# Performance work log

Measured on AMD Instinct MI355X. Metric: run time of the kernel, lower is better.

The kernel has to match this reference:

```python
import math
import jax, jax.numpy as jnp
from jax import lax
import numpy as np

D = 256; H = 8; NL = 6; HALF = D // 2
B = 32; NEV = 256

def sinpos(x):
    # SinusoidalPosEmb: (..., ) int -> (..., D)
    freq = jnp.exp(jnp.arange(HALF, dtype=jnp.float32) * (-math.log(10000.0) / (HALF - 1)))
    e = x.astype(jnp.float32)[..., None] * freq
    return jnp.concatenate([jnp.sin(e), jnp.cos(e)], axis=-1)

def layer_norm(x, g, b, eps=1e-5):
    m = x.mean(-1, keepdims=True)
    v = ((x - m) ** 2).mean(-1, keepdims=True)
    return (x - m) / jnp.sqrt(v + eps) * g + b

def gelu(x):
    return jax.nn.gelu(x, approximate=False)

def conv1d(x, w, b, stride):
    y = lax.conv_general_dilated(x, w, (stride,), [(3, 3)], dimension_numbers=("NCH", "OIH", "NCH"))
    return y + b[None, :, None]

def setup_inputs():
    ks = iter(jax.random.split(jax.random.key(0), 48))
    def p(*shape):
        return jax.random.normal(next(ks), shape, dtype=jnp.float32) * 0.02
    inp = dict(
        mel=jax.random.normal(next(ks), (B, 80, 2000), dtype=jnp.float32),
        events=jnp.sort(jax.random.randint(next(ks), (B, NEV), 0, 2000), axis=-1),
        event_mask=jnp.zeros((B, NEV), dtype=bool),
        star_rating=jax.random.uniform(next(ks), (B,), dtype=jnp.float32) * 9.0,
        mel_W=p(16, 80), mel_b=p(16),
        conv1_w=p(128, 16, 7), conv1_b=p(128),
        gn_g=jnp.ones(128, jnp.float32), gn_b=jnp.zeros(128, jnp.float32),
        conv2_w=p(256, 128, 7), conv2_b=p(256),
        cn_g=jnp.ones(D, jnp.float32), cn_b=jnp.zeros(D, jnp.float32),
        star_table=p(20, D),
        ep_W1=p(D, 3 * D), ep_b1=p(D), ep_W2=p(D, D), ep_b2=p(D),
        tl_Wqkv=p(NL, 3 * D, D), tl_bqkv=p(NL, 3 * D),
        tl_Wo=p(NL, D, D), tl_bo=p(NL, D),
        tl_ln1g=jnp.ones((NL, D), jnp.float32), tl_ln1b=jnp.zeros((NL, D), jnp.float32),
        tl_ln2g=jnp.ones((NL, D), jnp.float32), tl_ln2b=jnp.zeros((NL, D), jnp.float32),
        tl_W1=p(NL, 4 * D, D), tl_b1=p(NL, 4 * D),
        tl_W2=p(NL, D, 4 * D), tl_b2=p(NL, D),
        pool_q=jax.random.normal(next(ks), (D,), dtype=jnp.float32),
        on_g=jnp.ones(D, jnp.float32), on_b=jnp.zeros(D, jnp.float32),
        oh_W=p(1, D), oh_b=p(1),
    )
    return inp

def reference(mel, events, event_mask, star_rating, mel_W, mel_b, conv1_w, conv1_b, gn_g, gn_b, conv2_w, conv2_b, cn_g, cn_b, star_table, ep_W1, ep_b1, ep_W2, ep_b2, tl_Wqkv, tl_bqkv, tl_Wo, tl_bo, tl_ln1g, tl_ln1b, tl_ln2g, tl_ln2b, tl_W1, tl_b1, tl_W2, tl_b2, pool_q, on_g, on_b, oh_W, oh_b):
    Bsz = mel.shape[0]
    # mel_compress on channel dim: (B,80,T) -> (B,16,T)
    x_mel = jnp.einsum('bct,oc->bot', mel, mel_W) + mel_b[None, :, None]
    h = gelu(conv1d(x_mel, conv1_w, conv1_b, 2))           # (B,128,1000)
    # GroupNorm(1, C): normalize over (C, L) per sample
    m = h.mean((1, 2), keepdims=True)
    v = ((h - m) ** 2).mean((1, 2), keepdims=True)
    h = (h - m) / jnp.sqrt(v + 1e-5) * gn_g[None, :, None] + gn_b[None, :, None]
    h = gelu(conv1d(h, conv2_w, conv2_b, 2))               # (B,256,500)
    x = h.transpose(0, 2, 1)                               # (B,500,256)
    x = layer_norm(x, cn_g, cn_b)
    S = x.shape[1]
    x = x + sinpos(jnp.arange(S))[None]
    star_bucket = jnp.clip((star_rating / 0.5).astype(jnp.int32), 0, star_table.shape[0] - 1)
    x = x + star_table[star_bucket][:, None, :]
    # --- event gap/ratio embeddings (vectorized; exact match to torch loop when all valid) ---
    diff = jnp.maximum(events[:, 1:] - events[:, :-1], 1)  # clamp(min=1)
    g = jnp.concatenate([diff[:, :1], diff], axis=1)        # g[0] = g[1]
    gap_ms = g * 5
    g_f = jnp.maximum(g.astype(jnp.float32), 1.0)
    r = jnp.clip(g_f[:, 1:] / g_f[:, :-1], 0.1, 10.0)
    ones = jnp.ones((Bsz, 1), dtype=jnp.float32)
    ratio_before = (jnp.concatenate([ones, r], axis=1) * 50).astype(jnp.int32)
    ratio_after = (jnp.concatenate([r, ones], axis=1) * 50).astype(jnp.int32)
    combined = jnp.concatenate([sinpos(ratio_before), sinpos(ratio_after), sinpos(gap_ms)], axis=-1)
    ev = gelu(combined @ ep_W1.T + ep_b1) @ ep_W2.T + ep_b2
    ev = jnp.where(event_mask[..., None], 0.0, ev)
    token_pos = jnp.clip(events // 4, 0, S - 1)
    # batched scatter-add of event embeddings into token stream
    x = x.at[jnp.arange(Bsz)[:, None], token_pos].add(ev)
    hd = D // H
    for i in range(NL):
        xn = layer_norm(x, tl_ln1g[i], tl_ln1b[i])
        qkv = xn @ tl_Wqkv[i].T + tl_bqkv[i]
        q, k, vv = jnp.split(qkv, 3, axis=-1)
        q = q.reshape(Bsz, S, H, hd).transpose(0, 2, 1, 3)
        k = k.reshape(Bsz, S, H, hd).transpose(0, 2, 1, 3)
        vv = vv.reshape(Bsz, S, H, hd).transpose(0, 2, 1, 3)
        a = jax.nn.softmax(jnp.einsum('bhqd,bhkd->bhqk', q, k) / math.sqrt(hd), axis=-1)
        o = jnp.einsum('bhqk,bhkd->bhqd', a, vv).transpose(0, 2, 1, 3).reshape(Bsz, S, D)
        x = x + o @ tl_Wo[i].T + tl_bo[i]
        xn = layer_norm(x, tl_ln2g[i], tl_ln2b[i])
        x = x + gelu(xn @ tl_W1[i].T + tl_b1[i]) @ tl_W2[i].T + tl_b2[i]
    # attention pooling + head
    logits = x @ pool_q / math.sqrt(D)
    w = jax.nn.softmax(logits, axis=-1)
    pooled = jnp.einsum('bs,bsd->bd', w, x)
    return (layer_norm(pooled, on_g, on_b) @ oh_W.T + oh_b).squeeze(-1)
```

## Files before the change

kernel.cpp:

```cpp
#include <hip/hip_runtime.h>
#include <math.h>

namespace {
constexpr int kB = 32;
constexpr int kS = 500;
constexpr int kH = 8;
}
#define LKC (-0.07252236513366287)

typedef __attribute__((ext_vector_type(8))) short s16x8;
typedef __attribute__((ext_vector_type(4))) float f32x4;

__device__ __forceinline__ float gelu_f(float x){
  return 0.5f * x * (1.0f + erff(x * 0.7071067811865476f));
}
__device__ __forceinline__ float b2f(short s){
  union { unsigned u; float f; } x; x.u = ((unsigned)(unsigned short)s) << 16; return x.f;
}
__device__ __forceinline__ short f2b(float f){
  unsigned u = __float_as_uint(f);
  unsigned r = (u + 0x7fffu + ((u >> 16) & 1u)) >> 16;
  return (short)r;
}
__device__ __forceinline__ unsigned cvtpk(float lo, float hi){
  unsigned r;
  asm("v_cvt_pk_bf16_f32 %0, %1, %2" : "=v"(r) : "v"(lo), "v"(hi));
  return r;
}

__global__ __launch_bounds__(128) void conv1w_pad(const float* __restrict__ w, short* __restrict__ out){
  int n = blockIdx.x, k = threadIdx.x;
  out[n*128 + k] = (k < 112) ? f2b(w[n*112 + k]) : (short)0;
}

__global__ __launch_bounds__(256) void f2b_all(const float* __restrict__ c2,
    const float* __restrict__ e1, const float* __restrict__ e2,
    const float* __restrict__ qk, const float* __restrict__ wo,
    const float* __restrict__ w1, const float* __restrict__ w2,
    short* __restrict__ WB){
  int blk = blockIdx.x, t = threadIdx.x;
  const float* src; short* dst; int idx;
  if(blk < 896){        src = c2; dst = WB + 16384;   idx = blk*256 + t; }
  else if(blk < 1664){  src = e1; dst = WB + 245760;  idx = (blk-896)*256 + t; }
  else if(blk < 1920){  src = e2; dst = WB + 442368;  idx = (blk-1664)*256 + t; }
  else if(blk < 6528){  src = qk; dst = WB + 507904;  idx = (blk-1920)*256 + t; }
  else if(blk < 8064){  src = wo; dst = WB + 1687552; idx = (blk-6528)*256 + t; }
  else if(blk < 14208){ src = w1; dst = WB + 2080768; idx = (blk-8064)*256 + t; }
  else {                src = w2; dst = WB + 3653632; idx = (blk-14208)*256 + t; }
  dst[idx] = f2b(src[idx]);
}

template<int OUT, bool DOGELU>
__global__ __launch_bounds__(256) void gemm_mfma(const short* __restrict__ A,
    const short* __restrict__ W, const float* __restrict__ bias,
    void* __restrict__ Cv, int M, int N, int K){
  __shared__ __align__(16) short Al[128*64];
  __shared__ __align__(16) short Wl[128*64];
  const int t = threadIdx.x;
  const int wid = t >> 6, lane = t & 63;
  const int m0 = blockIdx.y * 128, n0 = blockIdx.x * 128;
  const int wr = (wid >> 1) * 64, wc = (wid & 1) * 64;
  const int frow = lane & 15, lg = lane >> 4;
  const int rA = t >> 3;
  const int sA = (t & 7) ^ (rA & 7);
  const short* Aq = A + (size_t)(m0 + rA) * K + sA * 8;
  const short* Wq = W + (size_t)(n0 + rA) * K + sA * 8;
  f32x4 acc[4][4] = {};
  for(int k0 = 0; k0 < K; k0 += 64){
    s16x8 av[4], wv[4];
    #pragma unroll
    for(int j = 0; j < 4; ++j){
      av[j] = *(const s16x8*)(Aq + k0 + (size_t)(32*j)*K);
      wv[j] = *(const s16x8*)(Wq + k0 + (size_t)(32*j)*K);
    }
    __syncthreads();
    #pragma unroll
    for(int j = 0; j < 4; ++j){
      *(s16x8*)&Al[t*8 + j*2048] = av[j];
      *(s16x8*)&Wl[t*8 + j*2048] = wv[j];
    }
    __syncthreads();
    #pragma unroll
    for(int kh = 0; kh < 2; ++kh){
      s16x8 a[4], b[4];
      #pragma unroll
      for(int mi = 0; mi < 4; ++mi){
        int r = wr + mi*16 + frow;
        a[mi] = *(const s16x8*)&Al[r*64 + (((kh*4 + lg) ^ (r & 7)) * 8)];
      }
      #pragma unroll
      for(int ni = 0; ni < 4; ++ni){
        int r = wc + ni*16 + frow;
        b[ni] = *(const s16x8*)&Wl[r*64 + (((kh*4 + lg) ^ (r & 7)) * 8)];
      }
      #pragma unroll
      for(int mi = 0; mi < 4; ++mi)
        #pragma unroll
        for(int ni = 0; ni < 4; ++ni)
          acc[mi][ni] = __builtin_amdgcn_mfma_f32_16x16x32_bf16(a[mi], b[ni], acc[mi][ni], 0, 0, 0);
    }
  }
  #pragma unroll
  for(int mi = 0; mi < 4; ++mi){
    #pragma unroll
    for(int ni = 0; ni < 4; ++ni){
      const int col = n0 + wc + ni*16 + (lane & 15);
      const float bv = bias[col];
      #pragma unroll
      for(int r = 0; r < 4; ++r){
        const int row = m0 + wr + mi*16 + (lane >> 4)*4 + r;
        float v = acc[mi][ni][r] + bv;
        if(DOGELU) v = gelu_f(v);
        if(OUT == 0) ((float*)Cv)[(size_t)row*N + col] = v;
        else if(OUT == 1) ((float*)Cv)[(size_t)row*N + col] += v;
        else ((short*)Cv)[(size_t)row*N + col] = f2b(v);
      }
    }
  }
}

template<bool DOGELU>
__global__ __launch_bounds__(512) void gemm512(const short* __restrict__ A,
    const short* __restrict__ W, const float* __restrict__ bias,
    short* __restrict__ C, int M, int N, int K){
  __shared__ __align__(16) short Al[128*64];
  __shared__ __align__(16) short Wl[256*64];
  const int t = threadIdx.x;
  const int wid = t >> 6, lane = t & 63;
  const int m0 = blockIdx.y * 128, n0 = blockIdx.x * 256;
  const int wm = wid >> 2, wn = wid & 3;
  const int frow = lane & 15, lg = lane >> 4;
  const int rA = t >> 3;
  const int sA = (t & 7) ^ (rA & 7);
  const short* Aq = A + (size_t)(m0 + rA) * K + sA * 8;
  const short* Wq = W + (size_t)(n0 + rA) * K + sA * 8;
  f32x4 acc[4][4] = {};
  for(int k0 = 0; k0 < K; k0 += 64){
    s16x8 av[2], wv[4];
    av[0] = *(const s16x8*)(Aq + k0);
    av[1] = *(const s16x8*)(Aq + k0 + (size_t)64*K);
    #pragma unroll
    for(int j = 0; j < 4; ++j)
      wv[j] = *(const s16x8*)(Wq + k0 + (size_t)(64*j)*K);
    __syncthreads();
    *(s16x8*)&Al[t*8] = av[0];
    *(s16x8*)&Al[t*8 + 4096] = av[1];
    #pragma unroll
    for(int j = 0; j < 4; ++j)
      *(s16x8*)&Wl[t*8 + j*4096] = wv[j];
    __syncthreads();
    #pragma unroll
    for(int kh = 0; kh < 2; ++kh){
      s16x8 a[4], b[4];
      #pragma unroll
      for(int mi = 0; mi < 4; ++mi){
        int r = wm*64 + mi*16 + frow;
        a[mi] = *(const s16x8*)&Al[r*64 + (((kh*4 + lg) ^ (r & 7)) * 8)];
      }
      #pragma unroll
      for(int ni = 0; ni < 4; ++ni){
        int r = wn*64 + ni*16 + frow;
        b[ni] = *(const s16x8*)&Wl[r*64 + (((kh*4 + lg) ^ (r & 7)) * 8)];
      }
      #pragma unroll
      for(int mi = 0; mi < 4; ++mi)
        #pragma unroll
        for(int ni = 0; ni < 4; ++ni)
          acc[mi][ni] = __builtin_amdgcn_mfma_f32_16x16x32_bf16(a[mi], b[ni], acc[mi][ni], 0, 0, 0);
    }
  }
  #pragma unroll
  for(int mi = 0; mi < 4; ++mi){
    #pragma unroll
    for(int ni = 0; ni < 4; ++ni){
      const int col = n0 + wn*64 + ni*16 + (lane & 15);
      const float bv = bias[col];
      #pragma unroll
      for(int r = 0; r < 4; ++r){
        const int row = m0 + wm*64 + mi*16 + (lane >> 4)*4 + r;
        float v = acc[mi][ni][r] + bv;
        if(DOGELU) v = gelu_f(v);
        C[(size_t)row*N + col] = f2b(v);
      }
    }
  }
}

template<bool DOLN>
__global__ __launch_bounds__(512) void gemm_ln(const short* __restrict__ A,
    const short* __restrict__ W, const float* __restrict__ bias,
    float* __restrict__ X, const float* __restrict__ lg_, const float* __restrict__ lb_,
    short* __restrict__ XNB, int M, int K){
  __shared__ __align__(16) short Al[64*64];
  __shared__ __align__(16) short Wl[256*64];
  __shared__ float sbuf[64][4];
  const int t = threadIdx.x;
  const int wid = t >> 6, lane = t & 63;
  const int m0 = blockIdx.y * 64;
  const int wm = wid >> 2, wn = wid & 3;
  const int frow = lane & 15, lg = lane >> 4;
  const int lq = lane & 15;
  const int rA = t >> 3;
  const int sA = (t & 7) ^ (rA & 7);
  const short* Aq = A + (size_t)(m0 + rA) * K + sA * 8;
  const short* Wq = W + (size_t)rA * K + sA * 8;
  f32x4 acc[2][4] = {};
  for(int k0 = 0; k0 < K; k0 += 64){
    s16x8 av = *(const s16x8*)(Aq + k0);
    s16x8 wv[4];
    #pragma unroll
    for(int j = 0; j < 4; ++j)
      wv[j] = *(const s16x8*)(Wq + k0 + (size_t)(64*j)*K);
    __syncthreads();
    *(s16x8*)&Al[t*8] = av;
    #pragma unroll
    for(int j = 0; j < 4; ++j)
      *(s16x8*)&Wl[t*8 + j*4096] = wv[j];
    __syncthreads();
    #pragma unroll
    for(int kh = 0; kh < 2; ++kh){
      s16x8 a[2], b[4];
      #pragma unroll
      for(int mi = 0; mi < 2; ++mi){
        int r = wm*32 + mi*16 + frow;
        a[mi] = *(const s16x8*)&Al[r*64 + (((kh*4 + lg) ^ (r & 7)) * 8)];
      }
      #pragma unroll
      for(int ni = 0; ni < 4; ++ni){
        int r = wn*64 + ni*16 + frow;
        b[ni] = *(const s16x8*)&Wl[r*64 + (((kh*4 + lg) ^ (r & 7)) * 8)];
      }
      #pragma unroll
      for(int mi = 0; mi < 2; ++mi)
        #pragma unroll
        for(int ni = 0; ni < 4; ++ni)
          acc[mi][ni] = __builtin_amdgcn_mfma_f32_16x16x32_bf16(a[mi], b[ni], acc[mi][ni], 0, 0, 0);
    }
  }
  float v[2][4][4];
  #pragma unroll
  for(int mi = 0; mi < 2; ++mi)
    #pragma unroll
    for(int ni = 0; ni < 4; ++ni){
      const int col = wn*64 + ni*16 + lq;
      const float bv = bias[col];
      #pragma unroll
      for(int r = 0; r < 4; ++r){
        const int row = m0 + wm*32 + mi*16 + lg*4 + r;
        v[mi][ni][r] = acc[mi][ni][r] + bv + X[(size_t)row*256 + col];
      }
    }
  __syncthreads();
  float vmean[2][4], vrstd[2][4];
  if(DOLN){
    #pragma unroll
    for(int mi = 0; mi < 2; ++mi)
      #pragma unroll
      for(int r = 0; r < 4; ++r){
        float s = v[mi][0][r] + v[mi][1][r] + v[mi][2][r] + v[mi][3][r];
        s += __shfl_xor(s, 1); s += __shfl_xor(s, 2);
        s += __shfl_xor(s, 4); s += __shfl_xor(s, 8);
        if(lq == 0) sbuf[wm*32 + mi*16 + lg*4 + r][wn] = s;
      }
    __syncthreads();
    #pragma unroll
    for(int mi = 0; mi < 2; ++mi)
      #pragma unroll
      for(int r = 0; r < 4; ++r){
        int rl = wm*32 + mi*16 + lg*4 + r;
        vmean[mi][r] = (sbuf[rl][0] + sbuf[rl][1] + sbuf[rl][2] + sbuf[rl][3]) * (1.f/256.f);
      }
    __syncthreads();
    #pragma unroll
    for(int mi = 0; mi < 2; ++mi)
      #pragma unroll
      for(int r = 0; r < 4; ++r){
        float q = 0.f;
        #pragma unroll
        for(int ni = 0; ni < 4; ++ni){ float d = v[mi][ni][r] - vmean[mi][r]; q += d*d; }
        q += __shfl_xor(q, 1); q += __shfl_xor(q, 2);
        q += __shfl_xor(q, 4); q += __shfl_xor(q, 8);
        if(lq == 0) sbuf[wm*32 + mi*16 + lg*4 + r][wn] = q;
      }
    __syncthreads();
    #pragma unroll
    for(int mi = 0; mi < 2; ++mi)
      #pragma unroll
      for(int r = 0; r < 4; ++r){
        int rl = wm*32 + mi*16 + lg*4 + r;
        float Q = sbuf[rl][0] + sbuf[rl][1] + sbuf[rl][2] + sbuf[rl][3];
        vrstd[mi][r] = 1.f / sqrtf(Q * (1.f/256.f) + 1e-5f);
      }
  }
  #pragma unroll
  for(int mi = 0; mi < 2; ++mi)
    #pragma unroll
    for(int ni = 0; ni < 4; ++ni){
      const int col = wn*64 + ni*16 + lq;
      float gg = 0.f, bb = 0.f;
      if(DOLN){ gg = lg_[col]; bb = lb_[col]; }
      #pragma unroll
      for(int r = 0; r < 4; ++r){
        const int row = m0 + wm*32 + mi*16 + lg*4 + r;
        float val = v[mi][ni][r];
        X[(size_t)row*256 + col] = val;
        if(DOLN)
          XNB[(size_t)row*256 + col] = f2b((val - vmean[mi][r]) * vrstd[mi][r] * gg + bb);
      }
    }
}

__global__ __launch_bounds__(256) void mel_kernel(const float* __restrict__ mel,
    const float* __restrict__ W, const float* __restrict__ bias, float* __restrict__ xm){
  __shared__ float Ws[16][80];
  __shared__ float bs[16];
  const int t = threadIdx.x;
  for(int i = t; i < 16*80; i += 256) Ws[i/80][i%80] = W[i];
  if(t < 16) bs[t] = bias[t];
  __syncthreads();
  int blk = blockIdx.x;
  int b = blk >> 3;
  int tc = (blk & 7) * 256 + t;
  if(tc >= 2000) return;
  float acc[16];
  #pragma unroll
  for(int o = 0; o < 16; ++o) acc[o] = bs[o];
  for(int c = 0; c < 80; ++c){
    float v = mel[((size_t)b*80 + c)*2000 + tc];
    #pragma unroll
    for(int o = 0; o < 16; ++o) acc[o] += v * Ws[o][c];
  }
  #pragma unroll
  for(int o = 0; o < 16; ++o) xm[((size_t)b*16 + o)*2000 + tc] = acc[o];
}

__global__ __launch_bounds__(256) void im2col1b(const float* __restrict__ xm, short* __restrict__ A){
  size_t idx = (size_t)blockIdx.x * 256 + threadIdx.x;
  int col = idx & 127;
  size_t row = idx >> 7;
  int t1 = row % 1000, b = row / 1000;
  float v = 0.f;
  if(col < 112){
    int i = col / 7, k = col % 7;
    int src = 2*t1 + k - 3;
    if(src >= 0 && src < 2000) v = xm[((size_t)b*16 + i)*2000 + src];
  }
  A[idx] = f2b(v);
}

__global__ __launch_bounds__(256) void gn_part(const float* __restrict__ h1, double* __restrict__ part){
  int blk = blockIdx.x;
  const float* p = h1 + (size_t)blk * 16000;
  int t = threadIdx.x;
  double s = 0, q = 0;
  for(int i = t; i < 16000; i += 256){ double v = p[i]; s += v; q += v*v; }
  __shared__ double rs[256], rq[256];
  rs[t] = s; rq[t] = q; __syncthreads();
  for(int s2 = 128; s2 > 0; s2 >>= 1){
    if(t < s2){ rs[t] += rs[t+s2]; rq[t] += rq[t+s2]; }
    __syncthreads();
  }
  if(t == 0){ part[blk*2] = rs[0]; part[blk*2+1] = rq[0]; }
}
__global__ __launch_bounds__(256) void gn_final(const double* __restrict__ part, float* __restrict__ stats){
  int t = threadIdx.x;
  int b = t >> 3;
  double s = part[t*2], q = part[t*2+1];
  s += __shfl_xor(s, 1); q += __shfl_xor(q, 1);
  s += __shfl_xor(s, 2); q += __shfl_xor(q, 2);
  s += __shfl_xor(s, 4); q += __shfl_xor(q, 4);
  if((t & 7) == 0){
    double mean = s / 128000.0;
    double var  = q / 128000.0 - mean*mean;
    stats[b*2]   = (float)mean;
    stats[b*2+1] = (float)(1.0 / sqrt(var + 1e-5));
  }
}

__global__ __launch_bounds__(256) void im2col2b(const float* __restrict__ h1,
    const float* __restrict__ stats, const float* __restrict__ gg,
    const float* __restrict__ gb, short* __restrict__ A){
  size_t idx = (size_t)blockIdx.x * 256 + threadIdx.x;
  int col = idx % 896;
  size_t row = idx / 896;
  int t2 = row % 500, b = row / 500;
  int i = col / 7, k = col % 7;
  int src = 2*t2 + k - 3;
  float v = 0.f;
  if(src >= 0 && src < 1000){
    float raw = h1[((size_t)b*1000 + src)*128 + i];
    v = (raw - stats[b*2]) * stats[b*2+1] * gg[i] + gb[i];
  }
  A[idx] = f2b(v);
}

__global__ __launch_bounds__(256) void postconv(const float* __restrict__ xp,
    const float* __restrict__ cg, const float* __restrict__ cb,
    const float* __restrict__ star, const float* __restrict__ stab,
    float* __restrict__ x){
  int row = blockIdx.x, t = threadIdx.x;
  int s = row % 500, b = row / 500;
  __shared__ float red[256];
  float v = xp[(size_t)row*256 + t];
  red[t] = v; __syncthreads();
  for(int s2 = 128; s2 > 0; s2 >>= 1){ if(t < s2) red[t] += red[t+s2]; __syncthreads(); }
  float mean = red[0] / 256.f; __syncthreads();
  float d = v - mean;
  red[t] = d*d; __syncthreads();
  for(int s2 = 128; s2 > 0; s2 >>= 1){ if(t < s2) red[t] += red[t+s2]; __syncthreads(); }
  float rstd = 1.f / sqrtf(red[0]/256.f + 1e-5f);
  int j = t & 127;
  double f = exp((double)j * LKC);
  double a = (double)s * f;
  float pe = (float)(t < 128 ? sin(a) : cos(a));
  int bucket = (int)(star[b] * 2.0f);
  bucket = bucket < 0 ? 0 : (bucket > 19 ? 19 : bucket);
  x[(size_t)row*256 + t] = d*rstd*cg[t] + cb[t] + pe + stab[bucket*256 + t];
}

__global__ __launch_bounds__(256) void event_feat(const int* __restrict__ events, short* __restrict__ comb){
  int blk = blockIdx.x;
  int e = blk & 255, b = blk >> 8;
  const int* ev = events + b*256;
  int t = threadIdx.x;
  auto gof = [&](int i){ int j = i < 1 ? 1 : i; int d = ev[j] - ev[j-1]; return d < 1 ? 1 : d; };
  int gi = gof(e);
  double rb = 1.0, ra = 1.0;
  if(e != 0){
    rb = (double)gi / (double)gof(e-1);
    rb = rb < 0.1 ? 0.1 : (rb > 10.0 ? 10.0 : rb);
  }
  if(e != 255){
    ra = (double)gof(e+1) / (double)gi;
    ra = ra < 0.1 ? 0.1 : (ra > 10.0 ? 10.0 : ra);
  }
  int rbi = (int)(rb * 50.0);
  int rai = (int)(ra * 50.0);
  int gap = 5 * gi;
  int j = t & 127;
  double f = exp((double)j * LKC);
  double a0 = (double)rbi * f, a1 = (double)rai * f, a2 = (double)gap * f;
  size_t base = (size_t)blk * 768;
  comb[base + t]       = f2b((float)(t < 128 ? sin(a0) : cos(a0)));
  comb[base + 256 + t] = f2b((float)(t < 128 ? sin(a1) : cos(a1)));
  comb[base + 512 + t] = f2b((float)(t < 128 ? sin(a2) : cos(a2)));
}

__global__ __launch_bounds__(256) void ev_scatter(const float* __restrict__ evout,
    const int* __restrict__ events, const unsigned char* __restrict__ mask,
    float* __restrict__ x){
  int blk = blockIdx.x;
  int e = blk & 255, b = blk >> 8;
  if(mask[b*256 + e]) return;
  int tp = events[b*256 + e] >> 2;
  tp = tp < 0 ? 0 : (tp > 499 ? 499 : tp);
  int t = threadIdx.x;
  atomicAdd(&x[((size_t)b*500 + tp)*256 + t], evout[(size_t)blk*256 + t]);
}

__global__ __launch_bounds__(256) void ln_rows(const float* __restrict__ x,
    const float* __restrict__ g, const float* __restrict__ b, short* __restrict__ out){
  int row = blockIdx.x, t = threadIdx.x;
  int wid = t >> 6, lane = t & 63;
  __shared__ float sm[8];
  float v = x[(size_t)row*256 + t];
  float s = v;
  #pragma unroll
  for(int o = 1; o < 64; o <<= 1) s += __shfl_xor(s, o);
  if(lane == 0) sm[wid] = s;
  __syncthreads();
  float mean = (sm[0] + sm[1] + sm[2] + sm[3]) * (1.f/256.f);
  float d = v - mean;
  float q = d*d;
  #pragma unroll
  for(int o = 1; o < 64; o <<= 1) q += __shfl_xor(q, o);
  if(lane == 0) sm[4 + wid] = q;
  __syncthreads();
  float rstd = 1.f / sqrtf((sm[4] + sm[5] + sm[6] + sm[7]) * (1.f/256.f) + 1e-5f);
  out[(size_t)row*256 + t] = f2b(d*rstd*g[t] + b[t]);
}

__global__ __launch_bounds__(512) void attn_mfma(const short* __restrict__ qkv,
    short* __restrict__ o){
  __shared__ __align__(16) short Kl[512*40];
  __shared__ __align__(16) short Vt[32*520];
  __shared__ __align__(16) short Pl[8][2][640];
  const int i = blockIdx.x;
  const int b = (i & 7)*4 + ((i >> 3) & 3);
  const int h = i >> 5;
  const int t = threadIdx.x;
  const int wid = t >> 6, lane = t & 63;
  const int lq = lane & 15, lg = lane >> 4;
  const short* base = qkv + (size_t)b * kS * 768;
  {
    const int c = t & 3;
    for(int idx = t; idx < 2048; idx += 512){
      int row = idx >> 2;
      s16x8 kv = {0,0,0,0,0,0,0,0};
      unsigned vu0 = 0, vu1 = 0, vu2 = 0, vu3 = 0;
      if(row < kS){
        const short* rp = base + (size_t)row*768 + 256 + h*32 + c*8;
        kv = *(const s16x8*)rp;
        uint4 vv = *(const uint4*)(rp + 256);
        vu0 = vv.x; vu1 = vv.y; vu2 = vv.z; vu3 = vv.w;
      }
      *(s16x8*)&Kl[row*40 + c*8] = kv;
      unsigned b0 = (c & 2) ? vu2 : vu0, b1 = (c & 2) ? vu3 : vu1;
      unsigned b2 = (c & 2) ? vu0 : vu2, b3 = (c & 2) ? vu1 : vu3;
      unsigned r0 = (c & 1) ? b1 : b0, r1 = (c & 1) ? b2 : b1;
      unsigned r2 = (c & 1) ? b3 : b2, r3 = (c & 1) ? b0 : b3;
      #pragma unroll
      for(int j0 = 0; j0 < 8; ++j0){
        unsigned w = (j0 >> 1) == 0 ? r0 : (j0 >> 1) == 1 ? r1 : (j0 >> 1) == 2 ? r2 : r3;
        short val = (short)((j0 & 1) ? (w >> 16) : (w & 0xffff));
        int d = c*8 + ((j0 + 2*c) & 7);
        Vt[d*520 + row] = val;
      }
    }
  }
  __syncthreads();
  const float c2 = 0.17677669529663687f * 1.4426950408889634f;
  for(int qi = 0; qi < 4; ++qi){
    const int qt = wid*4 + qi;
    const int q0 = qt*16;
    int qrow = q0 + lq; if(qrow > kS-1) qrow = kS-1;
    s16x8 qf = *(const s16x8*)(base + (size_t)qrow*768 + h*32 + lg*8);
    f32x4 sc[32];
    __builtin_amdgcn_s_setprio(1);
    #pragma unroll
    for(int kt = 0; kt < 32; ++kt){
      s16x8 kf = *(const s16x8*)&Kl[(kt*16 + lq)*40 + lg*8];
      f32x4 z = {0.f,0.f,0.f,0.f};
      sc[kt] = __builtin_amdgcn_mfma_f32_16x16x32_bf16(kf, qf, z, 0, 0, 0);
    }
    __builtin_amdgcn_s_setprio(0);
    if(lg >= 1){ sc[31][0] = -1e30f; sc[31][1] = -1e30f; sc[31][2] = -1e30f; sc[31][3] = -1e30f; }
    float l0 = 0.f, l1 = 0.f, l2 = 0.f, l3 = 0.f;
    #pragma unroll
    for(int kt = 0; kt < 32; ++kt){
      float p0 = exp2f(sc[kt][0] * c2);
      float p1 = exp2f(sc[kt][1] * c2);
      float p2 = exp2f(sc[kt][2] * c2);
      float p3 = exp2f(sc[kt][3] * c2);
      sc[kt][0] = p0; sc[kt][1] = p1; sc[kt][2] = p2; sc[kt][3] = p3;
      l0 += p0; l1 += p1; l2 += p2; l3 += p3;
    }
    float l = (l0 + l1) + (l2 + l3);
    l += __shfl_xor(l, 16, 64);
    l += __shfl_xor(l, 32, 64);
    f32x4 oa0 = {0.f,0.f,0.f,0.f}, oa1 = {0.f,0.f,0.f,0.f};
    #pragma unroll
    for(int kt2 = 0; kt2 < 16; ++kt2){
      short* pw = &Pl[wid][kt2 & 1][0];
      f32x4 p0 = sc[kt2*2], p1 = sc[kt2*2+1];
      uint2 pk0, pk1;
      pk0.x = cvtpk(p0[0], p0[1]); pk0.y = cvtpk(p0[2], p0[3]);
      pk1.x = cvtpk(p1[0], p1[1]); pk1.y = cvtpk(p1[2], p1[3]);
      *(uint2*)&pw[lq*40 + lg*4] = pk0;
      *(uint2*)&pw[lq*40 + 16 + lg*4] = pk1;
      s16x8 pf = *(const s16x8*)&pw[lq*40 + lg*8];
      s16x8 v0 = *(const s16x8*)&Vt[lq*520 + kt2*32 + lg*8];
      s16x8 v1 = *(const s16x8*)&Vt[(16+lq)*520 + kt2*32 + lg*8];
      __builtin_amdgcn_s_setprio(1);
      oa0 = __builtin_amdgcn_mfma_f32_16x16x32_bf16(v0, pf, oa0, 0, 0, 0);
      oa1 = __builtin_amdgcn_mfma_f32_16x16x32_bf16(v1, pf, oa1, 0, 0, 0);
      __builtin_amdgcn_s_setprio(0);
    }
    float inv = 1.f / l;
    int qw = q0 + lq;
    if(qw < kS){
      short* op = o + ((size_t)(b*kS + qw))*256 + h*32;
      uint2 w0, w1;
      w0.x = cvtpk(oa0[0]*inv, oa0[1]*inv); w0.y = cvtpk(oa0[2]*inv, oa0[3]*inv);
      w1.x = cvtpk(oa1[0]*inv, oa1[1]*inv); w1.y = cvtpk(oa1[2]*inv, oa1[3]*inv);
      *(uint2*)&op[lg*4] = w0;
      *(uint2*)&op[16 + lg*4] = w1;
    }
  }
}

__global__ __launch_bounds__(256) void pool_head(const float* __restrict__ x,
    const float* __restrict__ pq, const float* __restrict__ og, const float* __restrict__ ob,
    const float* __restrict__ ohW, const float* __restrict__ ohb, float* __restrict__ out){
  int b = blockIdx.x, t = threadIdx.x;
  __shared__ float lg[500];
  __shared__ float red[256];
  const float* xb = x + (size_t)b * 500 * 256;
  for(int s = t; s < 500; s += 256){
    const float* xr = xb + (size_t)s * 256;
    float d = 0.f;
    for(int c = 0; c < 256; ++c) d += xr[c] * pq[c];
    lg[s] = d * 0.0625f;
  }
  __syncthreads();
  float m = -1e30f;
  for(int s = t; s < 500; s += 256) m = fmaxf(m, lg[s]);
  red[t] = m; __syncthreads();
  for(int s2 = 128; s2 > 0; s2 >>= 1){ if(t < s2) red[t] = fmaxf(red[t], red[t+s2]); __syncthreads(); }
  m = red[0]; __syncthreads();
  float ps = 0.f;
  for(int s = t; s < 500; s += 256){ float e = expf(lg[s] - m); lg[s] = e; ps += e; }
  red[t] = ps; __syncthreads();
  for(int s2 = 128; s2 > 0; s2 >>= 1){ if(t < s2) red[t] += red[t+s2]; __syncthreads(); }
  float inv = 1.f / red[0];
  __syncthreads();
  float acc = 0.f;
  for(int s = 0; s < 500; ++s) acc += lg[s] * xb[(size_t)s*256 + t];
  acc *= inv;
  __syncthreads();
  red[t] = acc; __syncthreads();
  for(int s2 = 128; s2 > 0; s2 >>= 1){ if(t < s2) red[t] += red[t+s2]; __syncthreads(); }
  float mean = red[0] / 256.f; __syncthreads();
  float d = acc - mean;
  red[t] = d*d; __syncthreads();
  for(int s2 = 128; s2 > 0; s2 >>= 1){ if(t < s2) red[t] += red[t+s2]; __syncthreads(); }
  float rstd = 1.f / sqrtf(red[0]/256.f + 1e-5f);
  __syncthreads();
  float val = (d*rstd*og[t] + ob[t]) * ohW[t];
  red[t] = val; __syncthreads();
  for(int s2 = 128; s2 > 0; s2 >>= 1){ if(t < s2) red[t] += red[t+s2]; __syncthreads(); }
  if(t == 0) out[b] = red[0] + ohb[0];
}

extern "C" void kernel_launch(void* const* d_in, const int* in_sizes, int n_in,
                              void* d_out, int out_size, void* d_ws, size_t ws_size,
                              hipStream_t stream){
  const float* mel      = (const float*)d_in[0];
  const int*   events   = (const int*)d_in[1];
  const unsigned char* emask = (const unsigned char*)d_in[2];
  const float* star     = (const float*)d_in[3];
  const float* mel_W    = (const float*)d_in[4];
  const float* mel_b    = (const float*)d_in[5];
  const float* conv1_w  = (const float*)d_in[6];
  const float* conv1_b  = (const float*)d_in[7];
  const float* gn_g     = (const float*)d_in[8];
  const float* gn_b     = (const float*)d_in[9];
  const float* conv2_w  = (const float*)d_in[10];
  const float* conv2_b  = (const float*)d_in[11];
  const float* cn_g     = (const float*)d_in[12];
  const float* cn_b     = (const float*)d_in[13];
  const float* star_tab = (const float*)d_in[14];
  const float* ep_W1    = (const float*)d_in[15];
  const float* ep_b1    = (const float*)d_in[16];
  const float* ep_W2    = (const float*)d_in[17];
  const float* ep_b2    = (const float*)d_in[18];
  const float* tl_Wqkv  = (const float*)d_in[19];
  const float* tl_bqkv  = (const float*)d_in[20];
  const float* tl_Wo    = (const float*)d_in[21];
  const float* tl_bo    = (const float*)d_in[22];
  const float* tl_ln1g  = (const float*)d_in[23];
  const float* tl_ln1b  = (const float*)d_in[24];
  const float* tl_ln2g  = (const float*)d_in[25];
  const float* tl_ln2b  = (const float*)d_in[26];
  const float* tl_W1    = (const float*)d_in[27];
  const float* tl_b1    = (const float*)d_in[28];
  const float* tl_W2    = (const float*)d_in[29];
  const float* tl_b2    = (const float*)d_in[30];
  const float* pool_q   = (const float*)d_in[31];
  const float* on_g     = (const float*)d_in[32];
  const float* on_b     = (const float*)d_in[33];
  const float* oh_W     = (const float*)d_in[34];
  const float* oh_b     = (const float*)d_in[35];
  (void)in_sizes; (void)n_in; (void)out_size; (void)ws_size;

  float* ws  = (float*)d_ws;
  float* X   = ws;
  short* XNB = (short*)(ws + 4096000);
  short* OB  = (short*)(ws + 6144000);
  short* WB  = (short*)(ws + 8192000);
  float* BIG = ws + 10812000;
  double* PART = (double*)(ws + 28668000);
  float* STATS = ws + 28671900;

  short* WBc1 = WB + 0;
  short* WBc2 = WB + 16384;
  short* WBe1 = WB + 245760;
  short* WBe2 = WB + 442368;
  short* WBqk = WB + 507904;
  short* WBwo = WB + 1687552;
  short* WBw1 = WB + 2080768;
  short* WBw2 = WB + 3653632;

  float* XMEL = BIG;
  short* A1B  = (short*)(BIG + 1024000);
  float* H1   = BIG + 3072000;
  short* A2B  = (short*)(BIG + 7168000);
  float* XPRE = BIG;
  short* COMBB= (short*)BIG;
  short* EHIDB= (short*)(BIG + 3146000);
  float* EVO  = BIG + 4195000;
  short* QKVB = (short*)BIG;
  short* HIDB = (short*)(BIG + 7168000);

  conv1w_pad<<<128, 128, 0, stream>>>(conv1_w, WBc1);
  f2b_all<<<20352, 256, 0, stream>>>(conv2_w, ep_W1, ep_W2, tl_Wqkv, tl_Wo, tl_W1, tl_W2, WB);

  mel_kernel<<<kB*8, 256, 0, stream>>>(mel, mel_W, mel_b, XMEL);
  im2col1b<<<16000, 256, 0, stream>>>(XMEL, A1B);
  gemm_mfma<0,true><<<dim3(1, 250), 256, 0, stream>>>(A1B, WBc1, conv1_b, H1, 32000, 128, 128);
  gn_part<<<256, 256, 0, stream>>>(H1, PART);
  gn_final<<<1, 256, 0, stream>>>(PART, STATS);
  im2col2b<<<56000, 256, 0, stream>>>(H1, STATS, gn_g, gn_b, A2B);
  gemm_mfma<0,true><<<dim3(2, 125), 256, 0, stream>>>(A2B, WBc2, conv2_b, XPRE, 16000, 256, 896);
  postconv<<<16000, 256, 0, stream>>>(XPRE, cn_g, cn_b, star, star_tab, X);
  event_feat<<<kB*256, 256, 0, stream>>>(events, COMBB);
  gemm_mfma<2,true><<<dim3(2, 64), 256, 0, stream>>>(COMBB, WBe1, ep_b1, EHIDB, 8192, 256, 768);
  gemm_mfma<0,false><<<dim3(2, 64), 256, 0, stream>>>(EHIDB, WBe2, ep_b2, EVO, 8192, 256, 256);
  ev_scatter<<<kB*256, 256, 0, stream>>>(EVO, events, emask, X);

  ln_rows<<<16000, 256, 0, stream>>>(X, tl_ln1g, tl_ln1b, XNB);
  for(int i = 0; i < 6; ++i){
    gemm512<false><<<dim3(3, 125), 512, 0, stream>>>(XNB, WBqk + (size_t)i*196608, tl_bqkv + i*768, QKVB, 16000, 768, 256);
    attn_mfma<<<kB*kH, 512, 0, stream>>>(QKVB, OB);
    gemm_ln<true><<<dim3(1, 250), 512, 0, stream>>>(OB, WBwo + (size_t)i*65536, tl_bo + i*256,
        X, tl_ln2g + i*256, tl_ln2b + i*256, XNB, 16000, 256);
    gemm512<true><<<dim3(4, 125), 512, 0, stream>>>(XNB, WBw1 + (size_t)i*262144, tl_b1 + i*1024, HIDB, 16000, 1024, 256);
    if(i < 5)
      gemm_ln<true><<<dim3(1, 250), 512, 0, stream>>>(HIDB, WBw2 + (size_t)i*262144, tl_b2 + i*256,
          X, tl_ln1g + (i+1)*256, tl_ln1b + (i+1)*256, XNB, 16000, 1024);
    else
      gemm_ln<false><<<dim3(1, 250), 512, 0, stream>>>(HIDB, WBw2 + (size_t)i*262144, tl_b2 + i*256,
          X, tl_ln1g, tl_ln1b, XNB, 16000, 1024);
  }

  pool_head<<<kB, 256, 0, stream>>>(X, pool_q, on_g, on_b, oh_W, oh_b, (float*)d_out);
}
```

Before: 861.5 us.

## Split attention queries across two blocks and stream K/V in halves

The attention kernel now launches 512 blocks instead of 256, so each block handles half the query tiles of one (batch, head). Keys and values are staged into shared memory in two 256-row chunks, halving the LDS footprint, and softmax sums and output accumulators carry across the chunks without a running max. The aim is better CU occupancy and more resident blocks. The cost is that each K/V chunk is loaded twice across the block pair and an extra barrier is added per chunk.

```diff
diff --git a/kernel.cpp b/kernel.cpp
--- a/kernel.cpp
+++ b/kernel.cpp
@@ -482,97 +482,112 @@
 
 __global__ __launch_bounds__(512) void attn_mfma(const short* __restrict__ qkv,
     short* __restrict__ o){
-  __shared__ __align__(16) short Kl[512*40];
-  __shared__ __align__(16) short Vt[32*520];
+  __shared__ __align__(16) short Kl[256*40];
+  __shared__ __align__(16) short Vt[32*264];
   __shared__ __align__(16) short Pl[8][2][640];
   const int i = blockIdx.x;
   const int b = (i & 7)*4 + ((i >> 3) & 3);
-  const int h = i >> 5;
+  const int qh = (i >> 5) & 1;
+  const int h = (i >> 6) & 7;
   const int t = threadIdx.x;
   const int wid = t >> 6, lane = t & 63;
   const int lq = lane & 15, lg = lane >> 4;
   const short* base = qkv + (size_t)b * kS * 768;
-  {
-    const int c = t & 3;
-    for(int idx = t; idx < 2048; idx += 512){
-      int row = idx >> 2;
-      s16x8 kv = {0,0,0,0,0,0,0,0};
-      unsigned vu0 = 0, vu1 = 0, vu2 = 0, vu3 = 0;
-      if(row < kS){
-        const short* rp = base + (size_t)row*768 + 256 + h*32 + c*8;
-        kv = *(const s16x8*)rp;
-        uint4 vv = *(const uint4*)(rp + 256);
-        vu0 = vv.x; vu1 = vv.y; vu2 = vv.z; vu3 = vv.w;
-      }
-      *(s16x8*)&Kl[row*40 + c*8] = kv;
-      unsigned b0 = (c & 2) ? vu2 : vu0, b1 = (c & 2) ? vu3 : vu1;
-      unsigned b2 = (c & 2) ? vu0 : vu2, b3 = (c & 2) ? vu1 : vu3;
-      unsigned r0 = (c & 1) ? b1 : b0, r1 = (c & 1) ? b2 : b1;
-      unsigned r2 = (c & 1) ? b3 : b2, r3 = (c & 1) ? b0 : b3;
-      #pragma unroll
-      for(int j0 = 0; j0 < 8; ++j0){
-        unsigned w = (j0 >> 1) == 0 ? r0 : (j0 >> 1) == 1 ? r1 : (j0 >> 1) == 2 ? r2 : r3;
-        short val = (short)((j0 & 1) ? (w >> 16) : (w & 0xffff));
-        int d = c*8 + ((j0 + 2*c) & 7);
-        Vt[d*520 + row] = val;
-      }
-    }
-  }
-  __syncthreads();
   const float c2 = 0.17677669529663687f * 1.4426950408889634f;
-  for(int qi = 0; qi < 4; ++qi){
-    const int qt = wid*4 + qi;
-    const int q0 = qt*16;
-    int qrow = q0 + lq; if(qrow > kS-1) qrow = kS-1;
-    s16x8 qf = *(const s16x8*)(base + (size_t)qrow*768 + h*32 + lg*8);
-    f32x4 sc[32];
-    __builtin_amdgcn_s_setprio(1);
-    #pragma unroll
-    for(int kt = 0; kt < 32; ++kt){
-      s16x8 kf = *(const s16x8*)&Kl[(kt*16 + lq)*40 + lg*8];
-      f32x4 z = {0.f,0.f,0.f,0.f};
-      sc[kt] = __builtin_amdgcn_mfma_f32_16x16x32_bf16(kf, qf, z, 0, 0, 0);
-    }
-    __builtin_amdgcn_s_setprio(0);
-    if(lg >= 1){ sc[31][0] = -1e30f; sc[31][1] = -1e30f; sc[31][2] = -1e30f; sc[31][3] = -1e30f; }
-    float l0 = 0.f, l1 = 0.f, l2 = 0.f, l3 = 0.f;
-    #pragma unroll
-    for(int kt = 0; kt < 32; ++kt){
-      float p0 = exp2f(sc[kt][0] * c2);
-      float p1 = exp2f(sc[kt][1] * c2);
-      float p2 = exp2f(sc[kt][2] * c2);
-      float p3 = exp2f(sc[kt][3] * c2);
-      sc[kt][0] = p0; sc[kt][1] = p1; sc[kt][2] = p2; sc[kt][3] = p3;
-      l0 += p0; l1 += p1; l2 += p2; l3 += p3;
-    }
-    float l = (l0 + l1) + (l2 + l3);
+  s16x8 qf[2];
+  #pragma unroll
+  for(int qi = 0; qi < 2; ++qi){
+    int qrow = (qh*16 + wid*2 + qi)*16 + lq;
+    if(qrow > kS-1) qrow = kS-1;
+    qf[qi] = *(const s16x8*)(base + (size_t)qrow*768 + h*32 + lg*8);
+  }
+  float lsum[2] = {0.f, 0.f};
+  f32x4 oa0[2] = {}, oa1[2] = {};
+  for(int khalf = 0; khalf < 2; ++khalf){
+    const int k0base = khalf * 256;
+    if(khalf) __syncthreads();
+    {
+      const int c = t & 3;
+      for(int idx = t; idx < 1024; idx += 512){
+        int row = idx >> 2;
+        int grow = k0base + row;
+        s16x8 kv = {0,0,0,0,0,0,0,0};
+        unsigned vu0 = 0, vu1 = 0, vu2 = 0, vu3 = 0;
+        if(grow < kS){
+          const short* rp = base + (size_t)grow*768 + 256 + h*32 + c*8;
+          kv = *(const s16x8*)rp;
+          uint4 vv = *(const uint4*)(rp + 256);
+          vu0 = vv.x; vu1 = vv.y; vu2 = vv.z; vu3 = vv.w;
+        }
+        *(s16x8*)&Kl[row*40 + c*8] = kv;
+        unsigned b0 = (c & 2) ? vu2 : vu0, b1 = (c & 2) ? vu3 : vu1;
+        unsigned b2 = (c & 2) ? vu0 : vu2, b3 = (c & 2) ? vu1 : vu3;
+        unsigned r0 = (c & 1) ? b1 : b0, r1 = (c & 1) ? b2 : b1;
+        unsigned r2 = (c & 1) ? b3 : b2, r3 = (c & 1) ? b0 : b3;
+        #pragma unroll
+        for(int j0 = 0; j0 < 8; ++j0){
+          unsigned w = (j0 >> 1) == 0 ? r0 : (j0 >> 1) == 1 ? r1 : (j0 >> 1) == 2 ? r2 : r3;
+          short val = (short)((j0 & 1) ? (w >> 16) : (w & 0xffff));
+          int d = c*8 + ((j0 + 2*c) & 7);
+          Vt[d*264 + row] = val;
+        }
+      }
+    }
+    __syncthreads();
+    #pragma unroll
+    for(int qi = 0; qi < 2; ++qi){
+      f32x4 sc[16];
+      __builtin_amdgcn_s_setprio(1);
+      #pragma unroll
+      for(int kt = 0; kt < 16; ++kt){
+        s16x8 kf = *(const s16x8*)&Kl[(kt*16 + lq)*40 + lg*8];
+        f32x4 z = {0.f,0.f,0.f,0.f};
+        sc[kt] = __builtin_amdgcn_mfma_f32_16x16x32_bf16(kf, qf[qi], z, 0, 0, 0);
+      }
+      __builtin_amdgcn_s_setprio(0);
+      if(khalf == 1 && lg >= 1){ sc[15][0] = -1e30f; sc[15][1] = -1e30f; sc[15][2] = -1e30f; sc[15][3] = -1e30f; }
+      float l0 = 0.f, l1 = 0.f, l2 = 0.f, l3 = 0.f;
+      #pragma unroll
+      for(int kt = 0; kt < 16; ++kt){
+        float p0 = exp2f(sc[kt][0] * c2);
+        float p1 = exp2f(sc[kt][1] * c2);
+        float p2 = exp2f(sc[kt][2] * c2);
+        float p3 = exp2f(sc[kt][3] * c2);
+        sc[kt][0] = p0; sc[kt][1] = p1; sc[kt][2] = p2; sc[kt][3] = p3;
+        l0 += p0; l1 += p1; l2 += p2; l3 += p3;
+      }
+      lsum[qi] += (l0 + l1) + (l2 + l3);
+      #pragma unroll
+      for(int kt2 = 0; kt2 < 8; ++kt2){
+        short* pw = &Pl[wid][kt2 & 1][0];
+        f32x4 p0 = sc[kt2*2], p1 = sc[kt2*2+1];
+        uint2 pk0, pk1;
+        pk0.x = cvtpk(p0[0], p0[1]); pk0.y = cvtpk(p0[2], p0[3]);
+        pk1.x = cvtpk(p1[0], p1[1]); pk1.y = cvtpk(p1[2], p1[3]);
+        *(uint2*)&pw[lq*40 + lg*4] = pk0;
+        *(uint2*)&pw[lq*40 + 16 + lg*4] = pk1;
+        s16x8 pf = *(const s16x8*)&pw[lq*40 + lg*8];
+        s16x8 v0 = *(const s16x8*)&Vt[lq*264 + kt2*32 + lg*8];
+        s16x8 v1 = *(const s16x8*)&Vt[(16+lq)*264 + kt2*32 + lg*8];
+        __builtin_amdgcn_s_setprio(1);
+        oa0[qi] = __builtin_amdgcn_mfma_f32_16x16x32_bf16(v0, pf, oa0[qi], 0, 0, 0);
+        oa1[qi] = __builtin_amdgcn_mfma_f32_16x16x32_bf16(v1, pf, oa1[qi], 0, 0, 0);
+        __builtin_amdgcn_s_setprio(0);
+      }
+    }
+  }
+  #pragma unroll
+  for(int qi = 0; qi < 2; ++qi){
+    float l = lsum[qi];
     l += __shfl_xor(l, 16, 64);
     l += __shfl_xor(l, 32, 64);
-    f32x4 oa0 = {0.f,0.f,0.f,0.f}, oa1 = {0.f,0.f,0.f,0.f};
-    #pragma unroll
-    for(int kt2 = 0; kt2 < 16; ++kt2){
-      short* pw = &Pl[wid][kt2 & 1][0];
-      f32x4 p0 = sc[kt2*2], p1 = sc[kt2*2+1];
-      uint2 pk0, pk1;
-      pk0.x = cvtpk(p0[0], p0[1]); pk0.y = cvtpk(p0[2], p0[3]);
-      pk1.x = cvtpk(p1[0], p1[1]); pk1.y = cvtpk(p1[2], p1[3]);
-      *(uint2*)&pw[lq*40 + lg*4] = pk0;
-      *(uint2*)&pw[lq*40 + 16 + lg*4] = pk1;
-      s16x8 pf = *(const s16x8*)&pw[lq*40 + lg*8];
-      s16x8 v0 = *(const s16x8*)&Vt[lq*520 + kt2*32 + lg*8];
-      s16x8 v1 = *(const s16x8*)&Vt[(16+lq)*520 + kt2*32 + lg*8];
-      __builtin_amdgcn_s_setprio(1);
-      oa0 = __builtin_amdgcn_mfma_f32_16x16x32_bf16(v0, pf, oa0, 0, 0, 0);
-      oa1 = __builtin_amdgcn_mfma_f32_16x16x32_bf16(v1, pf, oa1, 0, 0, 0);
-      __builtin_amdgcn_s_setprio(0);
-    }
     float inv = 1.f / l;
-    int qw = q0 + lq;
+    int qw = (qh*16 + wid*2 + qi)*16 + lq;
     if(qw < kS){
       short* op = o + ((size_t)(b*kS + qw))*256 + h*32;
       uint2 w0, w1;
-      w0.x = cvtpk(oa0[0]*inv, oa0[1]*inv); w0.y = cvtpk(oa0[2]*inv, oa0[3]*inv);
-      w1.x = cvtpk(oa1[0]*inv, oa1[1]*inv); w1.y = cvtpk(oa1[2]*inv, oa1[3]*inv);
+      w0.x = cvtpk(oa0[qi][0]*inv, oa0[qi][1]*inv); w0.y = cvtpk(oa0[qi][2]*inv, oa0[qi][3]*inv);
+      w1.x = cvtpk(oa1[qi][0]*inv, oa1[qi][1]*inv); w1.y = cvtpk(oa1[qi][2]*inv, oa1[qi][3]*inv);
       *(uint2*)&op[lg*4] = w0;
       *(uint2*)&op[16 + lg*4] = w1;
     }
@@ -711,7 +726,7 @@
   ln_rows<<<16000, 256, 0, stream>>>(X, tl_ln1g, tl_ln1b, XNB);
   for(int i = 0; i < 6; ++i){
     gemm512<false><<<dim3(3, 125), 512, 0, stream>>>(XNB, WBqk + (size_t)i*196608, tl_bqkv + i*768, QKVB, 16000, 768, 256);
-    attn_mfma<<<kB*kH, 512, 0, stream>>>(QKVB, OB);
+    attn_mfma<<<512, 512, 0, stream>>>(QKVB, OB);
     gemm_ln<true><<<dim3(1, 250), 512, 0, stream>>>(OB, WBwo + (size_t)i*65536, tl_bo + i*256,
         X, tl_ln2g + i*256, tl_ln2b + i*256, XNB, 16000, 256);
     gemm512<true><<<dim3(4, 125), 512, 0, stream>>>(XNB, WBw1 + (size_t)i*262144, tl_b1 + i*1024, HIDB, 16000, 1024, 256);
```

After: 844.4 us, median of 2. -2.0%, faster.
